# Kernel optimization log

Hardware: AMD Instinct MI355X
Metric: run time of the kernel (lower is better)

## Reference

```python
import jax, jax.numpy as jnp
import numpy as np

D_MODEL = 32
N_HEADS = 4
D_K = 8
D_V = 8
LN_EPS = 1e-5
MASK_FILL = -1.0e9


def _layernorm(x, eps=LN_EPS):
    # torch.nn.LayerNorm with default affine params (gamma=1, beta=0)
    mu = jnp.mean(x, axis=-1, keepdims=True)
    var = jnp.var(x, axis=-1, keepdims=True)  # biased, matches torch
    return (x - mu) * jax.lax.rsqrt(var + eps)


def setup_inputs() -> dict:
    key = jax.random.key(0)
    ks = jax.random.split(key, 12)
    B, S = 8, 2048
    w = 1.0 / np.float32(np.sqrt(D_MODEL))
    return {
        "input_Q": jax.random.normal(ks[0], (B, S, D_MODEL), dtype=jnp.float32),
        "input_K": jax.random.normal(ks[1], (B, S, D_MODEL), dtype=jnp.float32),
        "input_V": jax.random.normal(ks[2], (B, S, D_MODEL), dtype=jnp.float32),
        "attn_mask": jax.random.randint(ks[3], (B, S, S), 0, 2).astype(jnp.bool_),
        "W_Q": jax.random.normal(ks[4], (D_MODEL, D_K * N_HEADS), dtype=jnp.float32) * w,
        "b_Q": jax.random.normal(ks[5], (D_K * N_HEADS,), dtype=jnp.float32) * 0.02,
        "W_K": jax.random.normal(ks[6], (D_MODEL, D_K * N_HEADS), dtype=jnp.float32) * w,
        "b_K": jax.random.normal(ks[7], (D_K * N_HEADS,), dtype=jnp.float32) * 0.02,
        "W_V": jax.random.normal(ks[8], (D_MODEL, D_V * N_HEADS), dtype=jnp.float32) * w,
        "b_V": jax.random.normal(ks[9], (D_V * N_HEADS,), dtype=jnp.float32) * 0.02,
        "W_O": jax.random.normal(ks[10], (D_V * N_HEADS, D_MODEL), dtype=jnp.float32) * w,
        "b_O": jax.random.normal(ks[11], (D_MODEL,), dtype=jnp.float32) * 0.02,
    }


def reference(input_Q, input_K, input_V, attn_mask, W_Q, b_Q, W_K, b_K, W_V, b_V, W_O, b_O):
    B, S, _ = input_Q.shape
    residual = input_Q
    # projections -> [B, H, S, d_head]
    Q = (input_Q @ W_Q + b_Q).reshape(B, S, N_HEADS, D_K).transpose(0, 2, 1, 3)
    K = (input_K @ W_K + b_K).reshape(B, S, N_HEADS, D_K).transpose(0, 2, 1, 3)
    V = (input_V @ W_V + b_V).reshape(B, S, N_HEADS, D_V).transpose(0, 2, 1, 3)
    scale = 1.0 / jnp.sqrt(jnp.asarray(D_K, dtype=Q.dtype))
    scores = jnp.einsum("bhqd,bhkd->bhqk", Q, K) * scale  # [B,H,S,S]
    scores = jnp.where(attn_mask[:, None, :, :], jnp.asarray(MASK_FILL, scores.dtype), scores)
    attn_ratio = jax.nn.softmax(scores, axis=-1)
    ctx = jnp.einsum("bhqk,bhkd->bhqd", attn_ratio, V)  # [B,H,S,Dv]
    self_attn = ctx.transpose(0, 2, 1, 3).reshape(B, S, N_HEADS * D_V)
    attn_output = self_attn @ W_O + b_O
    return (_layernorm(attn_output + residual), self_attn)
```

## Files before the change

### kernel.cpp

```cpp
#include <hip/hip_runtime.h>
#include <math.h>

#define D_MODEL 32
#define S_LEN   2048
#define B_SZ    8
#define NTOK    (B_SZ * S_LEN)
#define LN_EPS  1e-5f
#define LOG2E   1.44269504088896340736f
#define QK_SCALE 0.35355339059327373f
#define PROJ_BLKS (NTOK / 8)

typedef __attribute__((ext_vector_type(8)))  short    short8b;
typedef __attribute__((ext_vector_type(4)))  short    short4b;
typedef __attribute__((ext_vector_type(4)))  unsigned uint4v;
typedef __attribute__((ext_vector_type(16))) float    f32x16;

__device__ __forceinline__ unsigned short f2bf(float f) {
    unsigned u = __builtin_bit_cast(unsigned, f);
    unsigned r = (u + 0x7FFFu + ((u >> 16) & 1u)) >> 16;
    return (unsigned short)r;
}
__device__ __forceinline__ float bf2f(unsigned short h) {
    return __builtin_bit_cast(float, (unsigned)h << 16);
}
__device__ __forceinline__ unsigned cvtpk_bf16(float lo, float hi) {
    unsigned r;
    asm("v_cvt_pk_bf16_f32 %0, %1, %2" : "=v"(r) : "v"(lo), "v"(hi));
    return r;
}


__global__ __launch_bounds__(256) void prep_kernel(
    const void* __restrict__ mask,
    const float* __restrict__ xQ, const float* __restrict__ xK,
    const float* __restrict__ xV,
    const float* __restrict__ WQ, const float* __restrict__ bQ,
    const float* __restrict__ WK, const float* __restrict__ bK,
    const float* __restrict__ WV, const float* __restrict__ bV,
    unsigned short* __restrict__ QHC, unsigned short* __restrict__ QLC,
    unsigned short* __restrict__ KC,  unsigned short* __restrict__ VC,
    unsigned long long* __restrict__ pack)
{
    int bid = blockIdx.x;
    int t   = threadIdx.x;

    if (bid < 3 * PROJ_BLKS) {
        int which = bid / PROJ_BLKS;
        int xb    = bid - which * PROJ_BLKS;
        const float* x; const float* W; const float* bias; float scale;
        if (which == 0)      { x = xQ; W = WQ; bias = bQ; scale = QK_SCALE * LOG2E; }
        else if (which == 1) { x = xK; W = WK; bias = bK; scale = 1.0f; }
        else                 { x = xV; W = WV; bias = bV; scale = 1.0f; }

        __shared__ float xs[8][32];
        __shared__ float Ws[32][32];
        long base = (long)xb * 256;
        xs[t >> 5][t & 31] = x[base + t];
#pragma unroll
        for (int i = 0; i < 4; ++i) {
            int f = i * 256 + t;
            Ws[f >> 5][f & 31] = W[f];
        }
        __syncthreads();
        int r = t >> 5, j = t & 31;
        float acc = bias[j];
#pragma unroll
        for (int i = 0; i < 32; ++i) acc = fmaf(xs[r][i], Ws[i][j], acc);
        acc *= scale;

        long tok = (long)xb * 8 + r;
        long b   = tok >> 11;
        long ti  = tok & (S_LEN - 1);
        int  ch  = (int)(ti >> 5), kq = (int)(ti & 31);
        int  h   = j >> 3, d = j & 7;

        if (which == 0) {
            size_t qi = ((((size_t)b * 64 + ch) * 4 + h) * 32 + kq) * 8 + d;
            unsigned short hv = f2bf(acc);
            QHC[qi] = hv;
            QLC[qi] = f2bf(acc - bf2f(hv));
        } else if (which == 1) {
            size_t ki = (((((size_t)b * 64 + ch) * 4 + h) * 2 + 0) * 32 + kq) * 8 + d;
            unsigned short hv = f2bf(acc);
            KC[ki]       = hv;
            KC[ki + 256] = f2bf(acc - bf2f(hv));
        } else {
            size_t vi = (((size_t)b * 64 + ch) * 4 + h) * 256 + (size_t)d * 32 + kq;
            VC[vi] = f2bf(acc);
        }
    } else {
        int mb   = bid - 3 * PROJ_BLKS;
        long row = (long)mb * 4 + (t >> 6);
        int lane = t & 63;

        int probe = ((const int*)mask)[lane];
        bool is32 = (__ballot((probe & ~0xFF) == 0) == ~0ULL);

        unsigned long long* prow = pack + row * (S_LEN / 64);
        if (is32) {
            const int4* mr4 = (const int4*)((const int*)mask + row * S_LEN);
#pragma unroll
            for (int g = 0; g < 8; ++g) {
                int4 v = mr4[g * 64 + lane];
                unsigned long long b0 = __ballot(v.x != 0);
                unsigned long long b1 = __ballot(v.y != 0);
                unsigned long long b2 = __ballot(v.z != 0);
                unsigned long long b3 = __ballot(v.w != 0);
                if (lane == 0) {
                    prow[g * 4 + 0] = b0; prow[g * 4 + 1] = b1;
                    prow[g * 4 + 2] = b2; prow[g * 4 + 3] = b3;
                }
            }
        } else {
            const int* mri = (const int*)((const unsigned char*)mask + row * S_LEN);
#pragma unroll
            for (int g = 0; g < 8; ++g) {
                int v = mri[g * 64 + lane];
                unsigned long long b0 = __ballot((v & 0x000000FF) != 0);
                unsigned long long b1 = __ballot((v & 0x0000FF00) != 0);
                unsigned long long b2 = __ballot((v & 0x00FF0000) != 0);
                unsigned long long b3 = __ballot((v & 0xFF000000u) != 0);
                if (lane == 0) {
                    prow[g * 4 + 0] = b0; prow[g * 4 + 1] = b1;
                    prow[g * 4 + 2] = b2; prow[g * 4 + 3] = b3;
                }
            }
        }
    }
}

__global__ __launch_bounds__(512, 4) void attn_fused_kernel(
    const unsigned short* __restrict__ QHC, const unsigned short* __restrict__ QLC,
    const unsigned short* __restrict__ KC,  const unsigned short* __restrict__ VC,
    const unsigned long long* __restrict__ pack,
    const float* __restrict__ WO, const float* __restrict__ bO,
    const float* __restrict__ resid,
    float* __restrict__ sa_out, float* __restrict__ out0)
{
    constexpr int SEGLEN = 1024;
    constexpr int NGROUP = SEGLEN / 256;
    constexpr int NPT    = SEGLEN / 64;
    __shared__ float ctx_lds[2][32][33];
    __shared__ float l_lds[2][32][4];
    __shared__ float sa_lds[32][33];
    __shared__ float Ws[32][32];

    int raw  = blockIdx.x;
    int cid  = (raw & 7) * 64 + (raw >> 3);
    int b    = cid >> 6;
    int qt   = cid & 63;
    int tid  = threadIdx.x;
    int w    = tid >> 6;
    int h    = w & 3;
    int seg  = w >> 2;
    int lane = tid & 63;
    int q    = lane & 31;
    int half = lane >> 5;
    int tok0 = qt * 32;
    long tokq = (long)b * S_LEN + tok0 + q;
    int k0   = seg * SEGLEN;
    int ch0  = k0 >> 5;

    Ws[(tid >> 5) + ((tid & 31) >> 5) * 0][tid & 31] = 0.0f;
#pragma unroll
    for (int i = 0; i < 2; ++i) {
        int f = i * 512 + tid;
        Ws[f >> 5][f & 31] = WO[f];
    }

    f32x16 zero16;
#pragma unroll
    for (int i = 0; i < 16; ++i) zero16[i] = 0.0f;

    const unsigned long long* prow = pack + tokq * (S_LEN / 64);

    short ovv = (q == 8) ? (short)0x3F80 : (short)0;
    short8b ovf;
#pragma unroll
    for (int i = 0; i < 8; ++i) ovf[i] = ovv;

    size_t qoff = ((((size_t)b * 64 + qt) * 4 + h) * 32 + q) * 8;
    short8b qhf = *(const short8b*)(QHC + qoff);
    short8b qlf = *(const short8b*)(QLC + qoff);
    f32x16 cpv = zero16;

    const unsigned short* Kb0 = KC + (((size_t)b * 64) * 4 + h) * 512
                                   + (size_t)half * 256 + (size_t)q * 8;
    const unsigned short* Vb0 = VC + (((size_t)b * 64) * 4 + h) * 256
                                   + (size_t)q * 32 + half * 4;

    short8b kfA = *(const short8b*)(Kb0 + (size_t)ch0 * 2048);
    short8b kfB = *(const short8b*)(Kb0 + (size_t)(ch0 + 1) * 2048);
    short8b vf1c, vf2c;
    if (q < 8) {
        const unsigned short* vr = Vb0 + (size_t)ch0 * 1024;
        short4b a0 = *(const short4b*)(vr);
        short4b a1 = *(const short4b*)(vr + 8);
        short4b a2 = *(const short4b*)(vr + 16);
        short4b a3 = *(const short4b*)(vr + 24);
        vf1c = __builtin_shufflevector(a0, a1, 0, 1, 2, 3, 4, 5, 6, 7);
        vf2c = __builtin_shufflevector(a2, a3, 0, 1, 2, 3, 4, 5, 6, 7);
    } else { vf1c = ovf; vf2c = ovf; }

#pragma unroll
    for (int g = 0; g < NGROUP; ++g) {
        unsigned long long mg[4];
        mg[0] = prow[(k0 >> 6) + g * 4 + 0];
        mg[1] = prow[(k0 >> 6) + g * 4 + 1];
        mg[2] = prow[(k0 >> 6) + g * 4 + 2];
        mg[3] = prow[(k0 >> 6) + g * 4 + 3];

#pragma unroll 1
        for (int p = 0; p < 4; ++p) {
            int pa  = g * 4 + p;
            int chA = ch0 + 2 * pa;
            int chB = chA + 1;

            short8b kfA_n = kfA, kfB_n = kfB;
            if (pa + 1 < NPT) {
                kfA_n = *(const short8b*)(Kb0 + (size_t)(chA + 2) * 2048);
                kfB_n = *(const short8b*)(Kb0 + (size_t)(chB + 2) * 2048);
            }

            unsigned shA = (unsigned)(p * 16 + half);
            unsigned nA[4], nB[4];
#pragma unroll
            for (int c = 0; c < 4; ++c) {
                nA[c] = (unsigned)(mg[c] >> shA);
                nB[c] = (unsigned)(mg[c] >> (shA + 8u));
            }

            __builtin_amdgcn_s_setprio(1);
            f32x16 accA = __builtin_amdgcn_mfma_f32_32x32x16_bf16(kfA, qhf, zero16, 0, 0, 0);
            f32x16 accB = __builtin_amdgcn_mfma_f32_32x32x16_bf16(kfB, qhf, zero16, 0, 0, 0);
            accA = __builtin_amdgcn_mfma_f32_32x32x16_bf16(kfA, qlf, accA, 0, 0, 0);
            accB = __builtin_amdgcn_mfma_f32_32x32x16_bf16(kfB, qlf, accB, 0, 0, 0);
            __builtin_amdgcn_s_setprio(0);

            short8b vf1n, vf2n;
            if (q < 8) {
                const unsigned short* vr = Vb0 + (size_t)chB * 1024;
                short4b a0 = *(const short4b*)(vr);
                short4b a1 = *(const short4b*)(vr + 8);
                short4b a2 = *(const short4b*)(vr + 16);
                short4b a3 = *(const short4b*)(vr + 24);
                vf1n = __builtin_shufflevector(a0, a1, 0, 1, 2, 3, 4, 5, 6, 7);
                vf2n = __builtin_shufflevector(a2, a3, 0, 1, 2, 3, 4, 5, 6, 7);
            } else { vf1n = ovf; vf2n = ovf; }

            {
                unsigned pr[8];
#pragma unroll
                for (int j = 0; j < 8; ++j) {
                    const int c0 = (2 * j) & 3, c1 = (2 * j + 1) & 3;
                    const int s  = 2 * (j >> 1);
                    float p0 = ((nA[c0] >> s) & 1u) ? 0.0f
                             : __builtin_amdgcn_exp2f(accA[2 * j]);
                    float p1 = ((nA[c1] >> s) & 1u) ? 0.0f
                             : __builtin_amdgcn_exp2f(accA[2 * j + 1]);
                    pr[j] = cvtpk_bf16(p0, p1);
                }
                uint4v t1, t2;
                t1.x = pr[0]; t1.y = pr[1]; t1.z = pr[2]; t1.w = pr[3];
                t2.x = pr[4]; t2.y = pr[5]; t2.z = pr[6]; t2.w = pr[7];
                short8b pfa = __builtin_bit_cast(short8b, t1);
                short8b pfb = __builtin_bit_cast(short8b, t2);

                __builtin_amdgcn_s_setprio(1);
                cpv = __builtin_amdgcn_mfma_f32_32x32x16_bf16(vf1c, pfa, cpv, 0, 0, 0);
                cpv = __builtin_amdgcn_mfma_f32_32x32x16_bf16(vf2c, pfb, cpv, 0, 0, 0);
                __builtin_amdgcn_s_setprio(0);
            }

            short8b vf1nn, vf2nn;
            if (pa + 1 < NPT && q < 8) {
                const unsigned short* vr = Vb0 + (size_t)(chA + 2) * 1024;
                short4b a0 = *(const short4b*)(vr);
                short4b a1 = *(const short4b*)(vr + 8);
                short4b a2 = *(const short4b*)(vr + 16);
                short4b a3 = *(const short4b*)(vr + 24);
                vf1nn = __builtin_shufflevector(a0, a1, 0, 1, 2, 3, 4, 5, 6, 7);
                vf2nn = __builtin_shufflevector(a2, a3, 0, 1, 2, 3, 4, 5, 6, 7);
            } else { vf1nn = ovf; vf2nn = ovf; }

            {
                unsigned pr[8];
#pragma unroll
                for (int j = 0; j < 8; ++j) {
                    const int c0 = (2 * j) & 3, c1 = (2 * j + 1) & 3;
                    const int s  = 2 * (j >> 1);
                    float p0 = ((nB[c0] >> s) & 1u) ? 0.0f
                             : __builtin_amdgcn_exp2f(accB[2 * j]);
                    float p1 = ((nB[c1] >> s) & 1u) ? 0.0f
                             : __builtin_amdgcn_exp2f(accB[2 * j + 1]);
                    pr[j] = cvtpk_bf16(p0, p1);
                }
                uint4v t1, t2;
                t1.x = pr[0]; t1.y = pr[1]; t1.z = pr[2]; t1.w = pr[3];
                t2.x = pr[4]; t2.y = pr[5]; t2.z = pr[6]; t2.w = pr[7];
                short8b pfa = __builtin_bit_cast(short8b, t1);
                short8b pfb = __builtin_bit_cast(short8b, t2);

                __builtin_amdgcn_s_setprio(1);
                cpv = __builtin_amdgcn_mfma_f32_32x32x16_bf16(vf1n, pfa, cpv, 0, 0, 0);
                cpv = __builtin_amdgcn_mfma_f32_32x32x16_bf16(vf2n, pfb, cpv, 0, 0, 0);
                __builtin_amdgcn_s_setprio(0);
            }

            kfA = kfA_n;
            kfB = kfB_n;
            vf1c = vf1nn;
            vf2c = vf2nn;
        }
    }

    ctx_lds[seg][q][h * 8 + half * 4 + 0] = cpv[0];
    ctx_lds[seg][q][h * 8 + half * 4 + 1] = cpv[1];
    ctx_lds[seg][q][h * 8 + half * 4 + 2] = cpv[2];
    ctx_lds[seg][q][h * 8 + half * 4 + 3] = cpv[3];
    if (half == 0) l_lds[seg][q][h] = cpv[4];
    __syncthreads();

    int r = (tid >> 5) & 15;
    int j = tid & 31;
#pragma unroll
    for (int pass = 0; pass < 2; ++pass) {
        int tok = pass * 16 + r;
        float L  = l_lds[0][tok][j >> 3] + l_lds[1][tok][j >> 3];
        float cx = ctx_lds[0][tok][j] + ctx_lds[1][tok][j];
        float sa = cx / L;
        sa_lds[tok][j] = sa;
        sa_out[((long)b * S_LEN + tok0 + tok) * 32 + j] = sa;
    }
    __syncthreads();

#pragma unroll
    for (int pass = 0; pass < 2; ++pass) {
        int tok = pass * 16 + r;
        long grow = ((long)b * S_LEN + tok0 + tok) * 32;
        float y = bO[j] + resid[grow + j];
#pragma unroll
        for (int i = 0; i < 32; ++i) y = fmaf(sa_lds[tok][i], Ws[i][j], y);

        float sum = y;
#pragma unroll
        for (int o = 16; o >= 1; o >>= 1) sum += __shfl_xor(sum, o, 32);
        float mu = sum * (1.0f / 32.0f);
        float d  = y - mu;
        float sq = d * d;
#pragma unroll
        for (int o = 16; o >= 1; o >>= 1) sq += __shfl_xor(sq, o, 32);
        float var = sq * (1.0f / 32.0f);
        out0[grow + j] = d * rsqrtf(var + LN_EPS);
    }
}

extern "C" void kernel_launch(void* const* d_in, const int* in_sizes, int n_in,
                              void* d_out, int out_size, void* d_ws, size_t ws_size,
                              hipStream_t stream)
{
    const float* inQ = (const float*)d_in[0];
    const float* inK = (const float*)d_in[1];
    const float* inV = (const float*)d_in[2];
    const void*  mask = d_in[3];
    const float* WQ = (const float*)d_in[4];
    const float* bQ = (const float*)d_in[5];
    const float* WK = (const float*)d_in[6];
    const float* bK = (const float*)d_in[7];
    const float* WV = (const float*)d_in[8];
    const float* bV = (const float*)d_in[9];
    const float* WO = (const float*)d_in[10];
    const float* bO = (const float*)d_in[11];

    float* out0 = (float*)d_out;
    float* sa   = (float*)d_out + (long)NTOK * 32;

    char* ws = (char*)d_ws;
    unsigned short* QHC = (unsigned short*)(ws + 256);
    unsigned short* QLC = QHC + (size_t)NTOK * 32;
    unsigned short* KC  = QLC + (size_t)NTOK * 32;
    unsigned short* VC  = KC  + (size_t)NTOK * 64;
    unsigned long long* pack = (unsigned long long*)(VC + (size_t)NTOK * 32);

    prep_kernel<<<3 * PROJ_BLKS + NTOK / 4, 256, 0, stream>>>(
        mask, inQ, inK, inV, WQ, bQ, WK, bK, WV, bV, QHC, QLC, KC, VC, pack);

    attn_fused_kernel<<<B_SZ * 64, 512, 0, stream>>>(
        QHC, QLC, KC, VC, pack, WO, bO, inQ, sa, out0);
}
```

Baseline: 66.85 us.

## Fuse mask bit-packing into attention kernel with double-buffered LDS staging

Moves the boolean-mask to bitmask packing out of the prep kernel and into the attention kernel. Each group's mask bits are packed into a double-buffered LDS array while the current group is processed. This removes the global round trip of the packed mask and the extra prep blocks. The cost is raw mask reads inside the attention loop plus a block-wide barrier per group, which may stall the MFMA pipeline.

```diff
diff --git a/kernel.cpp b/kernel.cpp
--- a/kernel.cpp
+++ b/kernel.cpp
@@ -31,115 +31,73 @@
 
 
 __global__ __launch_bounds__(256) void prep_kernel(
-    const void* __restrict__ mask,
     const float* __restrict__ xQ, const float* __restrict__ xK,
     const float* __restrict__ xV,
     const float* __restrict__ WQ, const float* __restrict__ bQ,
     const float* __restrict__ WK, const float* __restrict__ bK,
     const float* __restrict__ WV, const float* __restrict__ bV,
     unsigned short* __restrict__ QHC, unsigned short* __restrict__ QLC,
-    unsigned short* __restrict__ KC,  unsigned short* __restrict__ VC,
-    unsigned long long* __restrict__ pack)
+    unsigned short* __restrict__ KC,  unsigned short* __restrict__ VC)
 {
     int bid = blockIdx.x;
     int t   = threadIdx.x;
 
-    if (bid < 3 * PROJ_BLKS) {
-        int which = bid / PROJ_BLKS;
-        int xb    = bid - which * PROJ_BLKS;
-        const float* x; const float* W; const float* bias; float scale;
-        if (which == 0)      { x = xQ; W = WQ; bias = bQ; scale = QK_SCALE * LOG2E; }
-        else if (which == 1) { x = xK; W = WK; bias = bK; scale = 1.0f; }
-        else                 { x = xV; W = WV; bias = bV; scale = 1.0f; }
-
-        __shared__ float xs[8][32];
-        __shared__ float Ws[32][32];
-        long base = (long)xb * 256;
-        xs[t >> 5][t & 31] = x[base + t];
-#pragma unroll
-        for (int i = 0; i < 4; ++i) {
-            int f = i * 256 + t;
-            Ws[f >> 5][f & 31] = W[f];
-        }
-        __syncthreads();
-        int r = t >> 5, j = t & 31;
-        float acc = bias[j];
-#pragma unroll
-        for (int i = 0; i < 32; ++i) acc = fmaf(xs[r][i], Ws[i][j], acc);
-        acc *= scale;
-
-        long tok = (long)xb * 8 + r;
-        long b   = tok >> 11;
-        long ti  = tok & (S_LEN - 1);
-        int  ch  = (int)(ti >> 5), kq = (int)(ti & 31);
-        int  h   = j >> 3, d = j & 7;
-
-        if (which == 0) {
-            size_t qi = ((((size_t)b * 64 + ch) * 4 + h) * 32 + kq) * 8 + d;
-            unsigned short hv = f2bf(acc);
-            QHC[qi] = hv;
-            QLC[qi] = f2bf(acc - bf2f(hv));
-        } else if (which == 1) {
-            size_t ki = (((((size_t)b * 64 + ch) * 4 + h) * 2 + 0) * 32 + kq) * 8 + d;
-            unsigned short hv = f2bf(acc);
-            KC[ki]       = hv;
-            KC[ki + 256] = f2bf(acc - bf2f(hv));
-        } else {
-            size_t vi = (((size_t)b * 64 + ch) * 4 + h) * 256 + (size_t)d * 32 + kq;
-            VC[vi] = f2bf(acc);
-        }
+    int which = bid / PROJ_BLKS;
+    int xb    = bid - which * PROJ_BLKS;
+    const float* x; const float* W; const float* bias; float scale;
+    if (which == 0)      { x = xQ; W = WQ; bias = bQ; scale = QK_SCALE * LOG2E; }
+    else if (which == 1) { x = xK; W = WK; bias = bK; scale = 1.0f; }
+    else                 { x = xV; W = WV; bias = bV; scale = 1.0f; }
+
+    __shared__ float xs[8][32];
+    __shared__ float Ws[32][32];
+    long base = (long)xb * 256;
+    xs[t >> 5][t & 31] = x[base + t];
+#pragma unroll
+    for (int i = 0; i < 4; ++i) {
+        int f = i * 256 + t;
+        Ws[f >> 5][f & 31] = W[f];
+    }
+    __syncthreads();
+    int r = t >> 5, j = t & 31;
+    float acc = bias[j];
+#pragma unroll
+    for (int i = 0; i < 32; ++i) acc = fmaf(xs[r][i], Ws[i][j], acc);
+    acc *= scale;
+
+    long tok = (long)xb * 8 + r;
+    long b   = tok >> 11;
+    long ti  = tok & (S_LEN - 1);
+    int  ch  = (int)(ti >> 5), kq = (int)(ti & 31);
+    int  h   = j >> 3, d = j & 7;
+
+    if (which == 0) {
+        size_t qi = ((((size_t)b * 64 + ch) * 4 + h) * 32 + kq) * 8 + d;
+        unsigned short hv = f2bf(acc);
+        QHC[qi] = hv;
+        QLC[qi] = f2bf(acc - bf2f(hv));
+    } else if (which == 1) {
+        size_t ki = (((((size_t)b * 64 + ch) * 4 + h) * 2 + 0) * 32 + kq) * 8 + d;
+        unsigned short hv = f2bf(acc);
+        KC[ki]       = hv;
+        KC[ki + 256] = f2bf(acc - bf2f(hv));
     } else {
-        int mb   = bid - 3 * PROJ_BLKS;
-        long row = (long)mb * 4 + (t >> 6);
-        int lane = t & 63;
-
-        int probe = ((const int*)mask)[lane];
-        bool is32 = (__ballot((probe & ~0xFF) == 0) == ~0ULL);
-
-        unsigned long long* prow = pack + row * (S_LEN / 64);
-        if (is32) {
-            const int4* mr4 = (const int4*)((const int*)mask + row * S_LEN);
-#pragma unroll
-            for (int g = 0; g < 8; ++g) {
-                int4 v = mr4[g * 64 + lane];
-                unsigned long long b0 = __ballot(v.x != 0);
-                unsigned long long b1 = __ballot(v.y != 0);
-                unsigned long long b2 = __ballot(v.z != 0);
-                unsigned long long b3 = __ballot(v.w != 0);
-                if (lane == 0) {
-                    prow[g * 4 + 0] = b0; prow[g * 4 + 1] = b1;
-                    prow[g * 4 + 2] = b2; prow[g * 4 + 3] = b3;
-                }
-            }
-        } else {
-            const int* mri = (const int*)((const unsigned char*)mask + row * S_LEN);
-#pragma unroll
-            for (int g = 0; g < 8; ++g) {
-                int v = mri[g * 64 + lane];
-                unsigned long long b0 = __ballot((v & 0x000000FF) != 0);
-                unsigned long long b1 = __ballot((v & 0x0000FF00) != 0);
-                unsigned long long b2 = __ballot((v & 0x00FF0000) != 0);
-                unsigned long long b3 = __ballot((v & 0xFF000000u) != 0);
-                if (lane == 0) {
-                    prow[g * 4 + 0] = b0; prow[g * 4 + 1] = b1;
-                    prow[g * 4 + 2] = b2; prow[g * 4 + 3] = b3;
-                }
-            }
-        }
+        size_t vi = (((size_t)b * 64 + ch) * 4 + h) * 256 + (size_t)d * 32 + kq;
+        VC[vi] = f2bf(acc);
     }
 }
 
 __global__ __launch_bounds__(512, 4) void attn_fused_kernel(
     const unsigned short* __restrict__ QHC, const unsigned short* __restrict__ QLC,
     const unsigned short* __restrict__ KC,  const unsigned short* __restrict__ VC,
-    const unsigned long long* __restrict__ pack,
+    const void* __restrict__ mask,
     const float* __restrict__ WO, const float* __restrict__ bO,
     const float* __restrict__ resid,
     float* __restrict__ sa_out, float* __restrict__ out0)
 {
     constexpr int SEGLEN = 1024;
-    constexpr int NGROUP = SEGLEN / 256;
     constexpr int NPT    = SEGLEN / 64;
+    __shared__ unsigned long long mpk[2][2][32][5];
     __shared__ float ctx_lds[2][32][33];
     __shared__ float l_lds[2][32][4];
     __shared__ float sa_lds[32][33];
@@ -157,22 +115,61 @@
     int q    = lane & 31;
     int half = lane >> 5;
     int tok0 = qt * 32;
-    long tokq = (long)b * S_LEN + tok0 + q;
+    long tokbase = (long)b * S_LEN + tok0;
+    long tokq    = tokbase + q;
     int k0   = seg * SEGLEN;
     int ch0  = k0 >> 5;
 
-    Ws[(tid >> 5) + ((tid & 31) >> 5) * 0][tid & 31] = 0.0f;
 #pragma unroll
     for (int i = 0; i < 2; ++i) {
         int f = i * 512 + tid;
         Ws[f >> 5][f & 31] = WO[f];
     }
 
+    int probe = ((const int*)mask)[lane];
+    bool is32 = (__ballot((probe & ~0xFF) == 0) == ~0ULL);
+
+    auto pack_group = [&](int g, int buf) {
+#pragma unroll
+        for (int i = 0; i < 4; ++i) {
+            int r = (w << 2) + i;
+            if (is32) {
+                const int4* rp = (const int4*)((const int*)mask
+                                               + (tokbase + r) * (long)S_LEN);
+#pragma unroll
+                for (int s2 = 0; s2 < 2; ++s2) {
+                    int4 v = rp[s2 * 256 + g * 64 + lane];
+                    unsigned long long b0 = __ballot(v.x != 0);
+                    unsigned long long b1 = __ballot(v.y != 0);
+                    unsigned long long b2 = __ballot(v.z != 0);
+                    unsigned long long b3 = __ballot(v.w != 0);
+                    if (lane == 0) {
+                        mpk[buf][s2][r][0] = b0; mpk[buf][s2][r][1] = b1;
+                        mpk[buf][s2][r][2] = b2; mpk[buf][s2][r][3] = b3;
+                    }
+                }
+            } else {
+                const int* rp = (const int*)((const unsigned char*)mask
+                                             + (tokbase + r) * (long)S_LEN);
+#pragma unroll
+                for (int s2 = 0; s2 < 2; ++s2) {
+                    int v = rp[s2 * 256 + g * 64 + lane];
+                    unsigned long long b0 = __ballot((v & 0x000000FF) != 0);
+                    unsigned long long b1 = __ballot((v & 0x0000FF00) != 0);
+                    unsigned long long b2 = __ballot((v & 0x00FF0000) != 0);
+                    unsigned long long b3 = __ballot((v & 0xFF000000u) != 0);
+                    if (lane == 0) {
+                        mpk[buf][s2][r][0] = b0; mpk[buf][s2][r][1] = b1;
+                        mpk[buf][s2][r][2] = b2; mpk[buf][s2][r][3] = b3;
+                    }
+                }
+            }
+        }
+    };
+
     f32x16 zero16;
 #pragma unroll
     for (int i = 0; i < 16; ++i) zero16[i] = 0.0f;
-
-    const unsigned long long* prow = pack + tokq * (S_LEN / 64);
 
     short ovv = (q == 8) ? (short)0x3F80 : (short)0;
     short8b ovf;
@@ -202,13 +199,20 @@
         vf2c = __builtin_shufflevector(a2, a3, 0, 1, 2, 3, 4, 5, 6, 7);
     } else { vf1c = ovf; vf2c = ovf; }
 
-#pragma unroll
-    for (int g = 0; g < NGROUP; ++g) {
+    pack_group(0, 0);
+    __syncthreads();
+
+#pragma unroll 1
+    for (int g = 0; g < 4; ++g) {
+        int cur = g & 1;
+
+        if (g + 1 < 4) pack_group(g + 1, cur ^ 1);
+
         unsigned long long mg[4];
-        mg[0] = prow[(k0 >> 6) + g * 4 + 0];
-        mg[1] = prow[(k0 >> 6) + g * 4 + 1];
-        mg[2] = prow[(k0 >> 6) + g * 4 + 2];
-        mg[3] = prow[(k0 >> 6) + g * 4 + 3];
+        mg[0] = mpk[cur][seg][q][0];
+        mg[1] = mpk[cur][seg][q][1];
+        mg[2] = mpk[cur][seg][q][2];
+        mg[3] = mpk[cur][seg][q][3];
 
 #pragma unroll 1
         for (int p = 0; p < 4; ++p) {
@@ -312,6 +316,8 @@
             vf1c = vf1nn;
             vf2c = vf2nn;
         }
+
+        __syncthreads();
     }
 
     ctx_lds[seg][q][h * 8 + half * 4 + 0] = cpv[0];
@@ -330,14 +336,14 @@
         float cx = ctx_lds[0][tok][j] + ctx_lds[1][tok][j];
         float sa = cx / L;
         sa_lds[tok][j] = sa;
-        sa_out[((long)b * S_LEN + tok0 + tok) * 32 + j] = sa;
+        sa_out[(tokbase + tok) * 32 + j] = sa;
     }
     __syncthreads();
 
 #pragma unroll
     for (int pass = 0; pass < 2; ++pass) {
         int tok = pass * 16 + r;
-        long grow = ((long)b * S_LEN + tok0 + tok) * 32;
+        long grow = (tokbase + tok) * 32;
         float y = bO[j] + resid[grow + j];
 #pragma unroll
         for (int i = 0; i < 32; ++i) y = fmaf(sa_lds[tok][i], Ws[i][j], y);
@@ -380,11 +386,10 @@
     unsigned short* QLC = QHC + (size_t)NTOK * 32;
     unsigned short* KC  = QLC + (size_t)NTOK * 32;
     unsigned short* VC  = KC  + (size_t)NTOK * 64;
-    unsigned long long* pack = (unsigned long long*)(VC + (size_t)NTOK * 32);
-
-    prep_kernel<<<3 * PROJ_BLKS + NTOK / 4, 256, 0, stream>>>(
-        mask, inQ, inK, inV, WQ, bQ, WK, bK, WV, bV, QHC, QLC, KC, VC, pack);
+
+    prep_kernel<<<3 * PROJ_BLKS, 256, 0, stream>>>(
+        inQ, inK, inV, WQ, bQ, WK, bK, WV, bV, QHC, QLC, KC, VC);
 
     attn_fused_kernel<<<B_SZ * 64, 512, 0, stream>>>(
-        QHC, QLC, KC, VC, pack, WO, bO, inQ, sa, out0);
-}
+        QHC, QLC, KC, VC, mask, WO, bO, inQ, sa, out0);
+}
```

Result: faster. 61.50 us (-8.0%).
